# Kernel tuning notes

Measured on AMD Instinct MI355X. Metric: run time of the kernel, lower is better.

Reference implementation:

```python
import jax, jax.numpy as jnp
import numpy as np

N_HEADS = 16

def setup_inputs() -> dict:
    key = jax.random.key(0)
    ks = jax.random.split(key, 6)
    B, S, D = 2, 2048, 1024
    sc = 0.02
    return {
        "x": jax.random.normal(ks[0], (B, S, D), dtype=jnp.float32),
        "Wq": jax.random.normal(ks[1], (D, D), dtype=jnp.float32) * sc,
        "Wk": jax.random.normal(ks[2], (D, D), dtype=jnp.float32) * sc,
        "Wv": jax.random.normal(ks[3], (D, D), dtype=jnp.float32) * sc,
        "Wo": jax.random.normal(ks[4], (D, D), dtype=jnp.float32) * sc,
        "bo": jnp.zeros((D,), dtype=jnp.float32),
        "stride": 64,
    }

def _strided_mask(S: int, stride: int):
    # local window |i-j|<=1  OR  |i-j| == k*stride (k>=1); diff==0 is in the window
    i = jnp.arange(S)[:, None]
    j = jnp.arange(S)[None, :]
    diff = jnp.abs(i - j)
    return (diff <= 1) | (diff % stride == 0)  # [S, S] bool

def reference(x, Wq, Wk, Wv, Wo, bo, stride):
    B, S, D = x.shape
    H = N_HEADS
    Dh = D // H
    # q/k/v projections: nn.Linear(bias=False) applies x @ W.T
    def proj(W):
        return (x @ W.T).reshape(B, S, H, Dh).transpose(0, 2, 1, 3)  # [B,H,S,Dh]
    q, k, v = proj(Wq), proj(Wk), proj(Wv)
    scores = jnp.einsum('bhqd,bhkd->bhqk', q, k) / jnp.sqrt(jnp.float32(Dh))
    mask = _strided_mask(S, stride)  # [S,S]
    scores = jnp.where(mask[None, None], scores, -jnp.inf)
    attn = jax.nn.softmax(scores, axis=-1)  # dropout is identity in eval
    out = jnp.einsum('bhqk,bhkd->bhqd', attn, v)  # [B,H,S,Dh]
    out = out.transpose(0, 2, 1, 3).reshape(B, S, D)
    return out @ Wo.T + bo
```

## Files before the change

kernel.cpp:

```cpp
#include <hip/hip_runtime.h>
#include <hip/hip_bf16.h>


typedef __bf16 bf16;
typedef __attribute__((ext_vector_type(4))) __bf16 bf16x4;
typedef __attribute__((ext_vector_type(8))) __bf16 bf16x8;
typedef __attribute__((ext_vector_type(4))) float f32x4;
typedef __attribute__((ext_vector_type(4))) unsigned int u32x4;

constexpr int S_ = 2048;
constexpr int D_ = 1024;
constexpr int H_ = 16;
constexpr int DH = 64;
constexpr int M_ = 2 * S_;

__device__ __forceinline__ void gload_lds16(const bf16* g, bf16* l) {
    __builtin_amdgcn_global_load_lds(
        (const __attribute__((address_space(1))) void*)g,
        (__attribute__((address_space(3))) void*)l, 16, 0, 0);
}

#define BARRIER_FULL() do { asm volatile("" ::: "memory"); \
    __builtin_amdgcn_sched_barrier(0); \
    __builtin_amdgcn_s_barrier(); \
    __builtin_amdgcn_sched_barrier(0); \
    asm volatile("" ::: "memory"); } while (0)

#define WAIT_LGKM0() do { asm volatile("s_waitcnt lgkmcnt(0)" ::: "memory"); \
    __builtin_amdgcn_sched_barrier(0); } while (0)

#define WAIT_VM0() do { asm volatile("s_waitcnt vmcnt(0)" ::: "memory"); \
    __builtin_amdgcn_sched_barrier(0); } while (0)

#define WAIT_VM4() do { asm volatile("s_waitcnt vmcnt(4)" ::: "memory"); \
    __builtin_amdgcn_sched_barrier(0); } while (0)

__device__ __forceinline__ void stage32(const bf16* __restrict__ G, int base_row,
                                        int kcol, bf16* lds, int wave, int lane)
{
    const int rIn = lane >> 2;
    const int g   = (lane & 3) ^ ((lane >> 2) & 3) ^ (lane >> 4);
    #pragma unroll
    for (int l = 0; l < 2; ++l) {
        const int R = (wave * 2 + l) * 16;
        gload_lds16(G + (size_t)(base_row + R + rIn) * D_ + kcol + g * 8,
                    lds + R * 32);
    }
}

__global__ __launch_bounds__(512, 1)
void gemm_qkv_p2(const bf16* __restrict__ A,
                 const bf16* __restrict__ W,
                 bf16* __restrict__ C)
{
    constexpr int BK = 32;
    constexpr int NT = D_ / BK;
    constexpr int TSLOT = 256 * BK;
    __shared__ __align__(16) bf16 As[3 * TSLOT];
    __shared__ __align__(16) bf16 Bs[3 * TSLOT];

    const int tid  = threadIdx.x;
    const int wave = tid >> 6;
    const int lane = tid & 63;
    const int wm = wave >> 2;
    const int wn = wave & 3;

    const int lid = blockIdx.y * 12 + blockIdx.x;
    const int xcd = lid & 7, pos = lid >> 3;
    const int bxs = (xcd & 1) * 6 + pos % 6;
    const int bys = (xcd >> 1) * 4 + pos / 6;
    const int bm = bys * 256;
    const int bn = bxs * 256;

    const int l15 = lane & 15;
    const int rs  = (lane >> 4) ^ (lane & 3) ^ ((lane >> 2) & 3);
    const int aRd = wm * 4096 + l15 * 32 + rs * 8;
    const int bRd = wn * 2048 + l15 * 32 + rs * 8;

    f32x4 acc[8][4];
    #pragma unroll
    for (int i = 0; i < 8; ++i)
        #pragma unroll
        for (int j = 0; j < 4; ++j) acc[i][j] = f32x4{0.f, 0.f, 0.f, 0.f};

    bf16x8 aF[4], bF[4];

#define READA_HALF(HH) do { _Pragma("unroll") \
    for (int fm = 0; fm < 4; ++fm) \
        aF[fm] = *(const bf16x8*)(aslot + aRd + (HH) * 2048 + fm * 512); \
    } while (0)

#define READB_ALL() do { _Pragma("unroll") \
    for (int fn = 0; fn < 4; ++fn) \
        bF[fn] = *(const bf16x8*)(bslot + bRd + fn * 512); \
    } while (0)

#define MFMA16(HH) do { _Pragma("unroll") \
    for (int fm = 0; fm < 4; ++fm) { _Pragma("unroll") \
        for (int fn = 0; fn < 4; ++fn) \
            acc[(HH) * 4 + fm][fn] = __builtin_amdgcn_mfma_f32_16x16x32_bf16( \
                aF[fm], bF[fn], acc[(HH) * 4 + fm][fn], 0, 0, 0); \
    } } while (0)

    stage32(A, bm, 0,  As,         wave, lane);
    stage32(W, bn, 0,  Bs,         wave, lane);
    stage32(A, bm, BK, As + TSLOT, wave, lane);
    stage32(W, bn, BK, Bs + TSLOT, wave, lane);
    WAIT_VM4();
    BARRIER_FULL();

    int cur = 0;
    for (int t = 0; t < NT; ++t) {
        const int ss = (cur + 2 >= 3) ? (cur - 1) : (cur + 2);
        const bf16* aslot = As + cur * TSLOT;
        const bf16* bslot = Bs + cur * TSLOT;
        const bool pre = (t + 2) < NT;
        const int kn = (t + 2) * BK;

        READB_ALL();
        READA_HALF(0);
        if (pre) stage32(A, bm, kn, As + ss * TSLOT, wave, lane);
        BARRIER_FULL(); WAIT_LGKM0();
        __builtin_amdgcn_s_setprio(1); MFMA16(0); __builtin_amdgcn_s_setprio(0);
        BARRIER_FULL();

        READA_HALF(1);
        if (pre) stage32(W, bn, kn, Bs + ss * TSLOT, wave, lane);
        BARRIER_FULL(); WAIT_LGKM0();
        __builtin_amdgcn_s_setprio(1); MFMA16(1); __builtin_amdgcn_s_setprio(0);
        if (pre) { WAIT_VM4(); } else { WAIT_VM0(); }
        BARRIER_FULL();

        cur = (cur + 1 >= 3) ? 0 : (cur + 1);
    }
#undef READA_HALF
#undef READB_ALL
#undef MFMA16

    #pragma unroll
    for (int fm8 = 0; fm8 < 8; ++fm8) {
        #pragma unroll
        for (int fn4 = 0; fn4 < 4; ++fn4) {
            const int n = bn + wn * 64 + fn4 * 16 + l15;
            const int z = n >> 10, col = n & 1023;
            bf16* Cz = C + (size_t)z * M_ * D_;
            const int mb = bm + wm * 128 + fm8 * 16 + (lane >> 4) * 4;
            #pragma unroll
            for (int r2 = 0; r2 < 4; ++r2)
                Cz[(size_t)(mb + r2) * D_ + col] = (bf16)acc[fm8][fn4][r2];
        }
    }
}

__device__ __forceinline__ void stage64(const bf16* __restrict__ G, int base_row,
                                        int kcol, bf16* lds, int wave, int lane)
{
    const int rIn = lane >> 3;
    const int g   = (lane & 7) ^ rIn;
    #pragma unroll
    for (int l = 0; l < 2; ++l) {
        const int c = wave * 2 + l;
        gload_lds16(G + (size_t)(base_row + c * 8 + rIn) * D_ + kcol + g * 8,
                    lds + c * 512);
    }
}

__global__ __launch_bounds__(512, 1)
void gemm_o_2ph(const bf16* __restrict__ A,
                const bf16* __restrict__ W,
                float* __restrict__ Cf,
                const float* __restrict__ bias)
{
    constexpr int BK = 64;
    constexpr int NT = D_ / BK;
    constexpr int TSLOT = 128 * BK;
    __shared__ __align__(16) bf16 As[3 * TSLOT];
    __shared__ __align__(16) bf16 Bs[3 * TSLOT];

    const int tid  = threadIdx.x;
    const int wave = tid >> 6;
    const int lane = tid & 63;
    const int wm = wave >> 2;
    const int wn = wave & 3;

    const int lid = blockIdx.y * 8 + blockIdx.x;
    const int xcd = lid & 7, pos = lid >> 3;
    const int bxs = (xcd & 3) * 2 + (pos & 1);
    const int bys = (xcd >> 2) * 16 + (pos >> 1);
    const int bm = bys * 128;
    const int bn = bxs * 128;

    const int l15 = lane & 15;
    const int hi  = lane >> 4;
    const int r7  = l15 & 7;

    int aOff[2][4], bOff[2][2];
    #pragma unroll
    for (int ks = 0; ks < 2; ++ks) {
        #pragma unroll
        for (int fm = 0; fm < 4; ++fm)
            aOff[ks][fm] = (wm * 64 + fm * 16 + l15) * 64 + (((ks * 4 + hi) ^ r7) * 8);
        #pragma unroll
        for (int fn = 0; fn < 2; ++fn)
            bOff[ks][fn] = (wn * 32 + fn * 16 + l15) * 64 + (((ks * 4 + hi) ^ r7) * 8);
    }

    f32x4 acc[4][2];
    #pragma unroll
    for (int i = 0; i < 4; ++i)
        #pragma unroll
        for (int j = 0; j < 2; ++j) acc[i][j] = f32x4{0.f, 0.f, 0.f, 0.f};

    bf16x8 aF[4], bF[2][2];

    stage64(A, bm, 0,  As,         wave, lane);
    stage64(W, bn, 0,  Bs,         wave, lane);
    stage64(A, bm, BK, As + TSLOT, wave, lane);
    stage64(W, bn, BK, Bs + TSLOT, wave, lane);
    WAIT_VM4();
    BARRIER_FULL();

    int cur = 0;
    for (int t = 0; t < NT; ++t) {
        const int ss = (cur + 2 >= 3) ? (cur - 1) : (cur + 2);
        const bf16* aslot = As + cur * TSLOT;
        const bf16* bslot = Bs + cur * TSLOT;
        const bool pre = (t + 2) < NT;
        const int kn = (t + 2) * BK;

        #pragma unroll
        for (int ks = 0; ks < 2; ++ks)
            #pragma unroll
            for (int fn = 0; fn < 2; ++fn)
                bF[ks][fn] = *(const bf16x8*)(bslot + bOff[ks][fn]);
        #pragma unroll
        for (int fm = 0; fm < 4; ++fm)
            aF[fm] = *(const bf16x8*)(aslot + aOff[0][fm]);
        if (pre) stage64(A, bm, kn, As + ss * TSLOT, wave, lane);
        BARRIER_FULL(); WAIT_LGKM0();
        __builtin_amdgcn_s_setprio(1);
        #pragma unroll
        for (int fm = 0; fm < 4; ++fm)
            #pragma unroll
            for (int fn = 0; fn < 2; ++fn)
                acc[fm][fn] = __builtin_amdgcn_mfma_f32_16x16x32_bf16(
                    aF[fm], bF[0][fn], acc[fm][fn], 0, 0, 0);
        __builtin_amdgcn_s_setprio(0);
        BARRIER_FULL();

        #pragma unroll
        for (int fm = 0; fm < 4; ++fm)
            aF[fm] = *(const bf16x8*)(aslot + aOff[1][fm]);
        if (pre) stage64(W, bn, kn, Bs + ss * TSLOT, wave, lane);
        BARRIER_FULL(); WAIT_LGKM0();
        __builtin_amdgcn_s_setprio(1);
        #pragma unroll
        for (int fm = 0; fm < 4; ++fm)
            #pragma unroll
            for (int fn = 0; fn < 2; ++fn)
                acc[fm][fn] = __builtin_amdgcn_mfma_f32_16x16x32_bf16(
                    aF[fm], bF[1][fn], acc[fm][fn], 0, 0, 0);
        __builtin_amdgcn_s_setprio(0);
        if (pre) { WAIT_VM4(); } else { WAIT_VM0(); }
        BARRIER_FULL();

        cur = (cur + 1 >= 3) ? 0 : (cur + 1);
    }

    #pragma unroll
    for (int fm = 0; fm < 4; ++fm) {
        #pragma unroll
        for (int fn = 0; fn < 2; ++fn) {
            const int n = bn + wn * 32 + fn * 16 + l15;
            const float bv = bias[n];
            const int mb = bm + wm * 64 + fm * 16 + hi * 4;
            #pragma unroll
            for (int r2 = 0; r2 < 4; ++r2)
                Cf[(size_t)(mb + r2) * D_ + n] = acc[fm][fn][r2] + bv;
        }
    }
}

template<bool AF32, bool BF32, bool CF32, bool BIAS>
__global__ __launch_bounds__(256)
void gemm_bt(const void* __restrict__ Av,
             const void* __restrict__ W0v, const void* __restrict__ W1v,
             const void* __restrict__ W2v,
             void* __restrict__ Cv, const float* __restrict__ bias)
{
    constexpr int BM = 128, BK = 64;
    constexpr int N = D_, K = D_;
    __shared__ __align__(16) bf16 As[BM * BK];
    __shared__ __align__(16) bf16 Bs[BM * BK];

    const int z = blockIdx.z;
    const void* Wv_ = (z == 0) ? W0v : (z == 1) ? W1v : W2v;

    const int tid  = threadIdx.x;
    const int wave = tid >> 6;
    const int lane = tid & 63;

    const int bm = blockIdx.y * BM;
    const int bn = blockIdx.x * BM;
    const int wr = wave >> 1;
    const int wc = wave & 1;

    f32x4 acc[4][4];
    #pragma unroll
    for (int i = 0; i < 4; ++i)
        #pragma unroll
        for (int j = 0; j < 4; ++j)
            acc[i][j] = f32x4{0.f, 0.f, 0.f, 0.f};

    const int ldRow = lane >> 3;
    const int ldCol = (lane & 7) * 8;

    for (int kt = 0; kt < K; kt += BK) {
        if (AF32) {
            const float* A = (const float*)Av;
            #pragma unroll
            for (int it = 0; it < 8; ++it) {
                const int flat = (it * 256 + tid) * 4;
                const int row = flat >> 6, col = flat & 63;
                const float4 v = *(const float4*)(A + (size_t)(bm + row) * K + kt + col);
                bf16x4 p = { (bf16)v.x, (bf16)v.y, (bf16)v.z, (bf16)v.w };
                *(bf16x4*)&As[row * BK + col] = p;
            }
        } else {
            const bf16* A = (const bf16*)Av;
            #pragma unroll
            for (int q = 0; q < 4; ++q) {
                const int c = wave * 4 + q;
                const int row = c * 8 + ldRow;
                gload_lds16(A + (size_t)(bm + row) * K + kt + ldCol, &As[c * 8 * BK]);
            }
        }
        if (BF32) {
            const float* W = (const float*)Wv_;
            #pragma unroll
            for (int it = 0; it < 8; ++it) {
                const int flat = (it * 256 + tid) * 4;
                const int row = flat >> 6, col = flat & 63;
                const float4 v = *(const float4*)(W + (size_t)(bn + row) * K + kt + col);
                bf16x4 p = { (bf16)v.x, (bf16)v.y, (bf16)v.z, (bf16)v.w };
                *(bf16x4*)&Bs[row * BK + col] = p;
            }
        } else {
            const bf16* W = (const bf16*)Wv_;
            #pragma unroll
            for (int q = 0; q < 4; ++q) {
                const int c = wave * 4 + q;
                const int row = c * 8 + ldRow;
                gload_lds16(W + (size_t)(bn + row) * K + kt + ldCol, &Bs[c * 8 * BK]);
            }
        }
        __syncthreads();
        #pragma unroll
        for (int kk = 0; kk < 2; ++kk) {
            const int k0 = kk * 32 + (lane >> 4) * 8;
            bf16x8 af[4], bfv[4];
            #pragma unroll
            for (int mi = 0; mi < 4; ++mi)
                af[mi] = *(const bf16x8*)&As[(wr * 64 + mi * 16 + (lane & 15)) * BK + k0];
            #pragma unroll
            for (int ni = 0; ni < 4; ++ni)
                bfv[ni] = *(const bf16x8*)&Bs[(wc * 64 + ni * 16 + (lane & 15)) * BK + k0];
            #pragma unroll
            for (int mi = 0; mi < 4; ++mi)
                #pragma unroll
                for (int ni = 0; ni < 4; ++ni)
                    acc[mi][ni] = __builtin_amdgcn_mfma_f32_16x16x32_bf16(
                        af[mi], bfv[ni], acc[mi][ni], 0, 0, 0);
        }
        __syncthreads();
    }

    #pragma unroll
    for (int mi = 0; mi < 4; ++mi) {
        #pragma unroll
        for (int ni = 0; ni < 4; ++ni) {
            const int n  = bn + wc * 64 + ni * 16 + (lane & 15);
            const int mb = bm + wr * 64 + mi * 16 + (lane >> 4) * 4;
            float bv = 0.f;
            if (BIAS) bv = bias[n];
            #pragma unroll
            for (int r2 = 0; r2 < 4; ++r2) {
                const int m = mb + r2;
                if (CF32) {
                    ((float*)Cv)[(size_t)m * N + n] = acc[mi][ni][r2] + bv;
                } else {
                    bf16* Cc = (bf16*)Cv + (size_t)z * M_ * D_;
                    Cc[(size_t)m * N + n] = (bf16)(acc[mi][ni][r2] + bv);
                }
            }
        }
    }
}

__global__ __launch_bounds__(256)
void convert_to_bf16(const float* __restrict__ x,
                     const float* __restrict__ w0, const float* __restrict__ w1,
                     const float* __restrict__ w2, const float* __restrict__ w3,
                     bf16* __restrict__ out)
{
    const size_t eid = ((size_t)blockIdx.x * 256 + threadIdx.x) * 8;
    const float* src; size_t off;
    if (eid < (size_t)(1u << 22)) { src = x; off = eid; }
    else {
        const size_t t = eid - (1u << 22);
        const int k = (int)(t >> 20);
        off = t & ((1u << 20) - 1);
        src = (k == 0) ? w0 : (k == 1) ? w1 : (k == 2) ? w2 : w3;
    }
    const float4 a = *(const float4*)(src + off);
    const float4 c = *(const float4*)(src + off + 4);
    bf16x8 v = { (bf16)a.x, (bf16)a.y, (bf16)a.z, (bf16)a.w,
                 (bf16)c.x, (bf16)c.y, (bf16)c.z, (bf16)c.w };
    *(bf16x8*)(out + eid) = v;
}

__device__ __forceinline__ unsigned pk2bf(float lo, float hi) {
    const unsigned a = __builtin_bit_cast(unsigned short, (bf16)lo);
    const unsigned b = __builtin_bit_cast(unsigned short, (bf16)hi);
    return a | (b << 16);
}

__global__ __launch_bounds__(256)
void attn_mfma(bf16* __restrict__ QA, const bf16* __restrict__ Kw,
               const bf16* __restrict__ Vw)
{
    const int lane = threadIdx.x & 63;
    const int wid  = blockIdx.x * 4 + (threadIdx.x >> 6);
    const int r = wid & 63;
    const int h = (wid >> 6) & (H_ - 1);
    const int b = wid >> 10;

    const int qlo = lane & 15;
    const int g   = lane >> 4;
    const size_t rb = (size_t)b * S_;
    const int col0 = h * DH;
    const float scale = 0.125f;

    f32x4 accS[2][2];
    #pragma unroll
    for (int a = 0; a < 2; ++a)
        #pragma unroll
        for (int c = 0; c < 2; ++c) accS[a][c] = f32x4{0.f,0.f,0.f,0.f};

    #pragma unroll
    for (int c = 0; c < 2; ++c) {
        bf16x8 kf[2], qf[2];
        #pragma unroll
        for (int t = 0; t < 2; ++t) {
            const size_t row = rb + (size_t)(r + 64 * (t * 16 + qlo));
            kf[t] = *(const bf16x8*)&Kw[row * D_ + col0 + c * 32 + g * 8];
            qf[t] = *(const bf16x8*)&QA[row * D_ + col0 + c * 32 + g * 8];
        }
        #pragma unroll
        for (int kt = 0; kt < 2; ++kt)
            #pragma unroll
            for (int qt = 0; qt < 2; ++qt)
                accS[kt][qt] = __builtin_amdgcn_mfma_f32_16x16x32_bf16(
                    kf[kt], qf[qt], accS[kt][qt], 0, 0, 0);
    }

    const int s_nb = lane & 31;
    const int side = lane >> 5;
    const int i_nb = r + 64 * s_nb;
    const int j_nb = side ? (i_nb + 1) : (i_nb - 1);
    const bool nbv = (unsigned)j_nb < (unsigned)S_;
    const int j_sf = nbv ? j_nb : i_nb;
    float nbd = 0.f;
    #pragma unroll
    for (int t = 0; t < 8; ++t) {
        const bf16x8 qv = *(const bf16x8*)&QA[(rb + i_nb) * D_ + col0 + t * 8];
        const bf16x8 kv = *(const bf16x8*)&Kw[(rb + j_sf) * D_ + col0 + t * 8];
        #pragma unroll
        for (int e = 0; e < 8; ++e) nbd += (float)qv[e] * (float)kv[e];
    }
    const float NEGINF = -__builtin_inff();
    float nb = nbv ? nbd * scale : NEGINF;

    float mx[2] = { NEGINF, NEGINF };
    #pragma unroll
    for (int kt = 0; kt < 2; ++kt)
        #pragma unroll
        for (int qt = 0; qt < 2; ++qt)
            #pragma unroll
            for (int rr = 0; rr < 4; ++rr)
                mx[qt] = fmaxf(mx[qt], accS[kt][qt][rr]);
    mx[0] *= scale; mx[1] *= scale;
    mx[g & 1] = fmaxf(mx[g & 1], nb);
    #pragma unroll
    for (int x = 16; x <= 32; x <<= 1) {
        mx[0] = fmaxf(mx[0], __shfl_xor(mx[0], x));
        mx[1] = fmaxf(mx[1], __shfl_xor(mx[1], x));
    }
    float p[2][2][4];
    float sm[2] = { 0.f, 0.f };
    #pragma unroll
    for (int kt = 0; kt < 2; ++kt)
        #pragma unroll
        for (int qt = 0; qt < 2; ++qt)
            #pragma unroll
            for (int rr = 0; rr < 4; ++rr) {
                const float e = __expf(accS[kt][qt][rr] * scale - mx[qt]);
                p[kt][qt][rr] = e;
                sm[qt] += e;
            }
    float nbp = __expf(nb - mx[g & 1]);
    sm[g & 1] += nbp;
    #pragma unroll
    for (int x = 16; x <= 32; x <<= 1) {
        sm[0] += __shfl_xor(sm[0], x);
        sm[1] += __shfl_xor(sm[1], x);
    }
    const float inv[2] = { 1.f / sm[0], 1.f / sm[1] };
    #pragma unroll
    for (int kt = 0; kt < 2; ++kt)
        #pragma unroll
        for (int qt = 0; qt < 2; ++qt)
            #pragma unroll
            for (int rr = 0; rr < 4; ++rr) p[kt][qt][rr] *= inv[qt];
    nbp *= inv[g & 1];

    unsigned pk_[2][2][2];
    #pragma unroll
    for (int qt = 0; qt < 2; ++qt)
        #pragma unroll
        for (int kt = 0; kt < 2; ++kt)
            #pragma unroll
            for (int w = 0; w < 2; ++w)
                pk_[qt][kt][w] = pk2bf(p[kt][qt][2 * w], p[kt][qt][2 * w + 1]);

    const int srcA = qlo + 32 * (g & 1);
    const int srcB = srcA + 16;
    const int kts  = g >> 1;
    bf16x8 pa[2];
    #pragma unroll
    for (int qt = 0; qt < 2; ++qt) {
        u32x4 fr;
        #pragma unroll
        for (int w = 0; w < 2; ++w) {
            const unsigned a0 = (unsigned)__shfl((int)pk_[qt][0][w], srcA);
            const unsigned a1 = (unsigned)__shfl((int)pk_[qt][1][w], srcA);
            fr[w] = kts ? a1 : a0;
            const unsigned b0 = (unsigned)__shfl((int)pk_[qt][0][w], srcB);
            const unsigned b1 = (unsigned)__shfl((int)pk_[qt][1][w], srcB);
            fr[2 + w] = kts ? b1 : b0;
        }
        pa[qt] = __builtin_bit_cast(bf16x8, fr);
    }

    f32x4 accO[2][4];
    #pragma unroll
    for (int qt = 0; qt < 2; ++qt)
        #pragma unroll
        for (int dt = 0; dt < 4; ++dt) accO[qt][dt] = f32x4{0.f,0.f,0.f,0.f};
    #pragma unroll
    for (int dt = 0; dt < 4; ++dt) {
        bf16x8 vf;
        #pragma unroll
        for (int e = 0; e < 8; ++e)
            vf[e] = Vw[(rb + (size_t)(r + 64 * (g * 8 + e))) * D_ + col0 + dt * 16 + qlo];
        accO[0][dt] = __builtin_amdgcn_mfma_f32_16x16x32_bf16(pa[0], vf, accO[0][dt], 0, 0, 0);
        accO[1][dt] = __builtin_amdgcn_mfma_f32_16x16x32_bf16(pa[1], vf, accO[1][dt], 0, 0, 0);
    }

    #pragma unroll
    for (int qt = 0; qt < 2; ++qt)
        #pragma unroll
        for (int rr = 0; rr < 4; ++rr) {
            const int q  = qt * 16 + g * 4 + rr;
            const int iq = r + 64 * q;
            const float pm = __shfl(nbp, q);
            const float pp = __shfl(nbp, q + 32);
            const int jm = iq > 0 ? iq - 1 : 0;
            const int jp = iq < S_ - 1 ? iq + 1 : S_ - 1;
            #pragma unroll
            for (int dt = 0; dt < 4; ++dt) {
                const int d = col0 + dt * 16 + qlo;
                const float vm = (float)Vw[(rb + jm) * D_ + d];
                const float vp = (float)Vw[(rb + jp) * D_ + d];
                const float o = accO[qt][dt][rr] + pm * vm + pp * vp;
                QA[(rb + iq) * D_ + d] = (bf16)o;
            }
        }
}

extern "C" void kernel_launch(void* const* d_in, const int* in_sizes, int n_in,
                              void* d_out, int out_size, void* d_ws, size_t ws_size,
                              hipStream_t stream)
{
    const float* x  = (const float*)d_in[0];
    const float* Wq = (const float*)d_in[1];
    const float* Wk = (const float*)d_in[2];
    const float* Wv = (const float*)d_in[3];
    const float* Wo = (const float*)d_in[4];
    const float* bo = (const float*)d_in[5];

    bf16* qws = (bf16*)d_ws;
    bf16* kws = qws + (size_t)M_ * D_;
    bf16* vws = kws + (size_t)M_ * D_;

    const bool fast = ws_size >= (size_t)40 * 1024 * 1024;

    if (fast) {
        bf16* xb  = vws + (size_t)M_ * D_;
        bf16* wqb = xb + (1u << 22);
        bf16* wob = wqb + 3 * (1u << 20);

        convert_to_bf16<<<4096, 256, 0, stream>>>(x, Wq, Wk, Wv, Wo, xb);

        gemm_qkv_p2<<<dim3(3 * D_ / 256, M_ / 256), 512, 0, stream>>>(xb, wqb, qws);

        attn_mfma<<<dim3(2 * H_ * 64 / 4), 256, 0, stream>>>(qws, kws, vws);

        gemm_o_2ph<<<dim3(D_ / 128, M_ / 128), 512, 0, stream>>>(
            qws, wob, (float*)d_out, bo);
    } else {
        gemm_bt<true, true, false, false><<<dim3(D_/128, M_/128, 3), 256, 0, stream>>>(
            x, Wq, Wk, Wv, qws, nullptr);

        attn_mfma<<<dim3(2 * H_ * 64 / 4), 256, 0, stream>>>(qws, kws, vws);

        gemm_bt<false, true, true, true><<<dim3(D_/128, M_/128, 1), 256, 0, stream>>>(
            qws, Wo, nullptr, nullptr, (float*)d_out, bo);
    }
}
```

Before: 87.07 us.

## Drop intra-iteration barriers and overlap second-half LDS reads with MFMAs in GEMMs

Restructures the main loop of the QKV and output-projection GEMMs. Both global-to-LDS prefetches for the stage two ahead are now issued at the top of each iteration, and three of the four block barriers per iteration are removed, leaving one. The second-half A fragments go into a separate register set and are read from LDS while the first-half MFMAs run, overlapping LDS latency with compute. This costs extra VGPRs for the duplicated A fragments and depends on the triple-buffered slots making the fewer barriers safe.

```diff
diff --git a/kernel.cpp b/kernel.cpp
--- a/kernel.cpp
+++ b/kernel.cpp
@@ -34,6 +34,8 @@
 
 #define WAIT_VM4() do { asm volatile("s_waitcnt vmcnt(4)" ::: "memory"); \
     __builtin_amdgcn_sched_barrier(0); } while (0)
+
+#define SCHED_FENCE() __builtin_amdgcn_sched_barrier(0)
 
 __device__ __forceinline__ void stage32(const bf16* __restrict__ G, int base_row,
                                         int kcol, bf16* lds, int wave, int lane)
@@ -83,24 +85,7 @@
         #pragma unroll
         for (int j = 0; j < 4; ++j) acc[i][j] = f32x4{0.f, 0.f, 0.f, 0.f};
 
-    bf16x8 aF[4], bF[4];
-
-#define READA_HALF(HH) do { _Pragma("unroll") \
-    for (int fm = 0; fm < 4; ++fm) \
-        aF[fm] = *(const bf16x8*)(aslot + aRd + (HH) * 2048 + fm * 512); \
-    } while (0)
-
-#define READB_ALL() do { _Pragma("unroll") \
-    for (int fn = 0; fn < 4; ++fn) \
-        bF[fn] = *(const bf16x8*)(bslot + bRd + fn * 512); \
-    } while (0)
-
-#define MFMA16(HH) do { _Pragma("unroll") \
-    for (int fm = 0; fm < 4; ++fm) { _Pragma("unroll") \
-        for (int fn = 0; fn < 4; ++fn) \
-            acc[(HH) * 4 + fm][fn] = __builtin_amdgcn_mfma_f32_16x16x32_bf16( \
-                aF[fm], bF[fn], acc[(HH) * 4 + fm][fn], 0, 0, 0); \
-    } } while (0)
+    bf16x8 aF0[4], aF1[4], bF[4];
 
     stage32(A, bm, 0,  As,         wave, lane);
     stage32(W, bn, 0,  Bs,         wave, lane);
@@ -115,27 +100,49 @@
         const bf16* aslot = As + cur * TSLOT;
         const bf16* bslot = Bs + cur * TSLOT;
         const bool pre = (t + 2) < NT;
-        const int kn = (t + 2) * BK;
-
-        READB_ALL();
-        READA_HALF(0);
-        if (pre) stage32(A, bm, kn, As + ss * TSLOT, wave, lane);
-        BARRIER_FULL(); WAIT_LGKM0();
-        __builtin_amdgcn_s_setprio(1); MFMA16(0); __builtin_amdgcn_s_setprio(0);
-        BARRIER_FULL();
-
-        READA_HALF(1);
-        if (pre) stage32(W, bn, kn, Bs + ss * TSLOT, wave, lane);
-        BARRIER_FULL(); WAIT_LGKM0();
-        __builtin_amdgcn_s_setprio(1); MFMA16(1); __builtin_amdgcn_s_setprio(0);
+
+        if (pre) {
+            const int kn = (t + 2) * BK;
+            stage32(A, bm, kn, As + ss * TSLOT, wave, lane);
+            stage32(W, bn, kn, Bs + ss * TSLOT, wave, lane);
+        }
+
+        #pragma unroll
+        for (int fn = 0; fn < 4; ++fn)
+            bF[fn] = *(const bf16x8*)(bslot + bRd + fn * 512);
+        #pragma unroll
+        for (int fm = 0; fm < 4; ++fm)
+            aF0[fm] = *(const bf16x8*)(aslot + aRd + fm * 512);
+        WAIT_LGKM0();
+
+        #pragma unroll
+        for (int fm = 0; fm < 4; ++fm)
+            aF1[fm] = *(const bf16x8*)(aslot + aRd + 2048 + fm * 512);
+        SCHED_FENCE();
+
+        __builtin_amdgcn_s_setprio(1);
+        #pragma unroll
+        for (int fm = 0; fm < 4; ++fm)
+            #pragma unroll
+            for (int fn = 0; fn < 4; ++fn)
+                acc[fm][fn] = __builtin_amdgcn_mfma_f32_16x16x32_bf16(
+                    aF0[fm], bF[fn], acc[fm][fn], 0, 0, 0);
+        __builtin_amdgcn_s_setprio(0);
+        WAIT_LGKM0();
+
+        __builtin_amdgcn_s_setprio(1);
+        #pragma unroll
+        for (int fm = 0; fm < 4; ++fm)
+            #pragma unroll
+            for (int fn = 0; fn < 4; ++fn)
+                acc[4 + fm][fn] = __builtin_amdgcn_mfma_f32_16x16x32_bf16(
+                    aF1[fm], bF[fn], acc[4 + fm][fn], 0, 0, 0);
+        __builtin_amdgcn_s_setprio(0);
+
         if (pre) { WAIT_VM4(); } else { WAIT_VM0(); }
         BARRIER_FULL();
-
         cur = (cur + 1 >= 3) ? 0 : (cur + 1);
     }
-#undef READA_HALF
-#undef READB_ALL
-#undef MFMA16
 
     #pragma unroll
     for (int fm8 = 0; fm8 < 8; ++fm8) {
@@ -211,7 +218,7 @@
         #pragma unroll
         for (int j = 0; j < 2; ++j) acc[i][j] = f32x4{0.f, 0.f, 0.f, 0.f};
 
-    bf16x8 aF[4], bF[2][2];
+    bf16x8 aF0[4], aF1[4], bF[2][2];
 
     stage64(A, bm, 0,  As,         wave, lane);
     stage64(W, bn, 0,  Bs,         wave, lane);
@@ -226,7 +233,12 @@
         const bf16* aslot = As + cur * TSLOT;
         const bf16* bslot = Bs + cur * TSLOT;
         const bool pre = (t + 2) < NT;
-        const int kn = (t + 2) * BK;
+
+        if (pre) {
+            const int kn = (t + 2) * BK;
+            stage64(A, bm, kn, As + ss * TSLOT, wave, lane);
+            stage64(W, bn, kn, Bs + ss * TSLOT, wave, lane);
+        }
 
         #pragma unroll
         for (int ks = 0; ks < 2; ++ks)
@@ -235,35 +247,35 @@
                 bF[ks][fn] = *(const bf16x8*)(bslot + bOff[ks][fn]);
         #pragma unroll
         for (int fm = 0; fm < 4; ++fm)
-            aF[fm] = *(const bf16x8*)(aslot + aOff[0][fm]);
-        if (pre) stage64(A, bm, kn, As + ss * TSLOT, wave, lane);
-        BARRIER_FULL(); WAIT_LGKM0();
+            aF0[fm] = *(const bf16x8*)(aslot + aOff[0][fm]);
+        WAIT_LGKM0();
+
+        #pragma unroll
+        for (int fm = 0; fm < 4; ++fm)
+            aF1[fm] = *(const bf16x8*)(aslot + aOff[1][fm]);
+        SCHED_FENCE();
+
         __builtin_amdgcn_s_setprio(1);
         #pragma unroll
         for (int fm = 0; fm < 4; ++fm)
             #pragma unroll
             for (int fn = 0; fn < 2; ++fn)
                 acc[fm][fn] = __builtin_amdgcn_mfma_f32_16x16x32_bf16(
-                    aF[fm], bF[0][fn], acc[fm][fn], 0, 0, 0);
+                    aF0[fm], bF[0][fn], acc[fm][fn], 0, 0, 0);
         __builtin_amdgcn_s_setprio(0);
-        BARRIER_FULL();
-
-        #pragma unroll
-        for (int fm = 0; fm < 4; ++fm)
-            aF[fm] = *(const bf16x8*)(aslot + aOff[1][fm]);
-        if (pre) stage64(W, bn, kn, Bs + ss * TSLOT, wave, lane);
-        BARRIER_FULL(); WAIT_LGKM0();
+        WAIT_LGKM0();
+
         __builtin_amdgcn_s_setprio(1);
         #pragma unroll
         for (int fm = 0; fm < 4; ++fm)
             #pragma unroll
             for (int fn = 0; fn < 2; ++fn)
                 acc[fm][fn] = __builtin_amdgcn_mfma_f32_16x16x32_bf16(
-                    aF[fm], bF[1][fn], acc[fm][fn], 0, 0, 0);
+                    aF1[fm], bF[1][fn], acc[fm][fn], 0, 0, 0);
         __builtin_amdgcn_s_setprio(0);
+
         if (pre) { WAIT_VM4(); } else { WAIT_VM0(); }
         BARRIER_FULL();
-
         cur = (cur + 1 >= 3) ? 0 : (cur + 1);
     }
 
```

New measurement: 97.53 us. +12.0%, slower.
